# Kernel tuning notes

Measured on AMD Instinct MI355X. Metric: run time of the kernel, lower is better.

Reference implementation:

```python
import jax, jax.numpy as jnp
import numpy as np

K = 5  # Chebyshev order


def laplacian(w):
    # normalized Laplacian: I - D^{-1/2} W D^{-1/2}
    d = jnp.sum(w, axis=1)
    d_re = 1.0 / jnp.sqrt(d + 1e-5)
    return jnp.eye(w.shape[0], dtype=w.dtype) - d_re[:, None] * w * d_re[None, :]


def cheb_terms(x, lap, k):
    # x: [B,N,C], lap: [N,N] -> [B,k,N,C]
    # Faithful to torch code: T0 = ones, then (x, lap@x) recurrence for k>2.
    t0 = jnp.ones_like(x)
    if k == 1:
        return t0[:, None]
    t1 = jnp.matmul(lap, x)
    if k == 2:
        return jnp.stack([t0, t1], axis=1)
    terms = [t0, x, t1]
    tkm1, tk = x, t1
    for _ in range(3, k):
        tkm1, tk = tk, 2.0 * jnp.matmul(lap, tk) - tkm1
        terms.append(tk)
    return jnp.stack(terms, axis=1)


def graph_conv(x, lap, w, k):
    # torch: cp.permute(0,2,3,1).flatten(2) @ w, i.e. flat index = c*k + t
    t = cheb_terms(x, lap, k)                       # [B,k,N,C]
    C = x.shape[-1]
    O = w.shape[-1]
    return jnp.einsum('bknc,cko->bno', t, w.reshape(C, k, O))


def setup_inputs() -> dict:
    key = jax.random.key(0)
    ks = jax.random.split(key, 9)
    B, N, Cin, H = 8192, 32, 60, 128
    return {
        'x': jax.random.normal(ks[0], (B, N, Cin), dtype=jnp.float32),
        'adj': jax.random.normal(ks[1], (N, N), dtype=jnp.float32) * 0.1,
        'adj_bias': jax.random.normal(ks[2], (1,), dtype=jnp.float32) * 0.1 + 0.2,
        'w1': jax.random.normal(ks[3], (K * Cin, H), dtype=jnp.float32) * 0.05,
        'b1': jax.random.normal(ks[4], (1, 1, H), dtype=jnp.float32) * 0.05,
        'w2': jax.random.normal(ks[5], (K * H, H), dtype=jnp.float32) * 0.05,
        'b2': jax.random.normal(ks[6], (1, 1, H), dtype=jnp.float32) * 0.05,
        'fc_w': jax.random.normal(ks[7], (2, N * H), dtype=jnp.float32) * 0.02,
        'fc_b': jax.random.normal(ks[8], (2,), dtype=jnp.float32) * 0.02,
    }


def reference(x, adj, adj_bias, w1, b1, w2, b2, fc_w, fc_b):
    # DGCNN.forward (eval mode: dropout = identity)
    a = jax.nn.relu(adj + adj_bias)
    lap = laplacian(a)
    h = graph_conv(x, lap, w1, K)
    h = jax.nn.relu(h + b1)      # B1ReLU
    h = graph_conv(h, lap, w2, K)
    h = jax.nn.relu(h + b2)
    h = h.reshape(h.shape[0], -1)  # [B, N*H]
    return h @ fc_w.T + fc_b
```

## Files before the change

### kernel.cpp

```cpp
#include <hip/hip_runtime.h>

typedef unsigned short u16;
typedef unsigned int u32;
typedef short bf16x8 __attribute__((ext_vector_type(8)));
typedef float f32x4 __attribute__((ext_vector_type(4)));

#define MFMA16(a, b, c) __builtin_amdgcn_mfma_f32_16x16x32_bf16((a), (b), (c), 0, 0, 0)

__device__ __forceinline__ u16 f2bf(float f) {
  u32 u = __builtin_bit_cast(u32, f);
  u += 0x7FFFu + ((u >> 16) & 1u);
  return (u16)(u >> 16);
}
__device__ __forceinline__ u32 pk2bf(float a, float b) {
#if __has_builtin(__builtin_amdgcn_cvt_pk_bf16_f32)
  auto v = __builtin_amdgcn_cvt_pk_bf16_f32(a, b);
  return __builtin_bit_cast(u32, v);
#else
  return (u32)f2bf(a) | ((u32)f2bf(b) << 16);
#endif
}

#define WS_MGF   0
#define WS_WT1F  8192
#define WS_WT2F  73728
#define WS_B1    204800
#define WS_B2    205312

__global__ void prep_kernel(const float* __restrict__ adj,
                            const float* __restrict__ adj_bias,
                            const float* __restrict__ w1,
                            const float* __restrict__ b1,
                            const float* __restrict__ w2,
                            const float* __restrict__ b2,
                            char* __restrict__ ws) {
  const int tid = threadIdx.x;
  if (blockIdx.x == 0) {
    __shared__ float sa[1024], Ls[1024], L2s[1024], L3s[1024], sdre[32];
    float bias = adj_bias[0];
    for (int i = tid; i < 1024; i += 256) sa[i] = fmaxf(adj[i] + bias, 0.0f);
    __syncthreads();
    if (tid < 32) {
      float s = 0.0f;
      for (int c = 0; c < 32; ++c) s += sa[tid * 32 + c];
      sdre[tid] = 1.0f / sqrtf(s + 1e-5f);
    }
    __syncthreads();
    for (int i = tid; i < 1024; i += 256) {
      int n = i >> 5, c = i & 31;
      Ls[i] = (n == c ? 1.0f : 0.0f) - sdre[n] * sa[i] * sdre[c];
    }
    __syncthreads();
    for (int i = tid; i < 1024; i += 256) {
      int r = i >> 5, c = i & 31;
      float s = 0.0f;
      for (int m = 0; m < 32; ++m) s += Ls[r * 32 + m] * Ls[m * 32 + c];
      L2s[i] = s;
    }
    __syncthreads();
    for (int i = tid; i < 1024; i += 256) {
      int r = i >> 5, c = i & 31;
      float s = 0.0f;
      for (int m = 0; m < 32; ++m) s += L2s[r * 32 + m] * Ls[m * 32 + c];
      L3s[i] = s;
    }
    __syncthreads();
    u16* MGf = (u16*)(ws + WS_MGF);
    for (int i = tid; i < 4096; i += 256) {
      int jt = i >> 9, lane = (i >> 3) & 63, j = i & 7;
      int col = jt * 16 + (lane & 15);
      int k = ((lane >> 4) << 3) + j;
      int kk = col >> 5, np = col & 31;
      float v;
      if (kk == 0)      v = (np == k) ? 1.0f : 0.0f;
      else if (kk == 1) v = Ls[np * 32 + k];
      else if (kk == 2) v = 2.0f * L2s[np * 32 + k] - (np == k ? 1.0f : 0.0f);
      else              v = 4.0f * L3s[np * 32 + k] - 3.0f * Ls[np * 32 + k];
      MGf[i] = f2bf(v);
    }
    float* B1 = (float*)(ws + WS_B1);
    float* B2 = (float*)(ws + WS_B2);
    if (tid < 128) {
      float s = b1[tid];
      for (int c = 0; c < 60; ++c) s += w1[(c * 5) * 128 + tid];
      B1[tid] = s;
    } else {
      int o = tid - 128;
      float s = b2[o];
      for (int c = 0; c < 128; ++c) s += w2[(c * 5) * 128 + o];
      B2[o] = s;
    }
  } else {
    u16* WT1F = (u16*)(ws + WS_WT1F);
    u16* WT2F = (u16*)(ws + WS_WT2F);
    int g = (blockIdx.x - 1) * 256 + tid;
    for (int i = g; i < 32768; i += 16 * 256) {
      int ot = i >> 12, ks = (i >> 9) & 7, lane = (i >> 3) & 63, j = i & 7;
      int o = ot * 16 + (lane & 15);
      int kc = ks * 32 + ((lane >> 4) << 3) + j;
      int k = kc >> 6, c = kc & 63;
      WT1F[i] = (c < 60) ? f2bf(w1[(c * 5 + k + 1) * 128 + o]) : (u16)0;
    }
    for (int i = g; i < 65536; i += 16 * 256) {
      int mt = i >> 13, h = (i >> 12) & 1, ks = (i >> 9) & 7;
      int lane = (i >> 3) & 63, j = i & 7;
      int kc = ((ks >> 1) << 7) + ((ks & 1) << 5) + (h << 6) + (((lane >> 4)) << 3) + j;
      int k = kc >> 7, c = kc & 127;
      int o = (mt << 4) + (lane & 15);
      WT2F[i] = f2bf(w2[(c * 5 + k + 1) * 128 + o]);
    }
  }
}

__global__ __launch_bounds__(256, 5) void dgcnn_kernel(
    const float* __restrict__ x,
    const char* __restrict__ ws,
    const float* __restrict__ fc_w,
    const float* __restrict__ fc_b,
    float* __restrict__ out) {
  __shared__ __align__(16) char arena[27136];
  __shared__ float red[8];
  u16* Xt = (u16*)arena;
  u16* Ht = (u16*)arena;
  u16* Y  = (u16*)(arena + 10240);

  const u16* MGf  = (const u16*)(ws + WS_MGF);
  const u16* WT1F = (const u16*)(ws + WS_WT1F);
  const u16* WT2F = (const u16*)(ws + WS_WT2F);
  const float* bias1 = (const float*)(ws + WS_B1);
  const float* bias2 = (const float*)(ws + WS_B2);

  const int tid = threadIdx.x;
  const int w = tid >> 6, lane = tid & 63;
  const int l15 = lane & 15, q = lane >> 4;
  const int b = blockIdx.x;
  const f32x4 z4 = {0.0f, 0.0f, 0.0f, 0.0f};

  for (int i = tid; i < 160; i += 256) Xt[(60 + (i / 40)) * 40 + (i % 40)] = 0;
  bf16x8 mB0 = *(const bf16x8*)(MGf + ((2 * w + 0) * 64 + lane) * 8);
  bf16x8 mB1 = *(const bf16x8*)(MGf + ((2 * w + 1) * 64 + lane) * 8);
  const float* xb = x + (size_t)b * 1920;
  for (int i = tid; i < 1920; i += 256) {
    int n = i / 60, c = i - n * 60;
    Xt[c * 40 + n] = f2bf(xb[i]);
  }
  __syncthreads();

  {
    f32x4 acc[4][2];
#pragma unroll
    for (int mt = 0; mt < 4; ++mt) {
      bf16x8 aX = *(const bf16x8*)&Xt[(mt * 16 + l15) * 40 + q * 8];
      acc[mt][0] = MFMA16(aX, mB0, z4);
      acc[mt][1] = MFMA16(aX, mB1, z4);
    }
    __syncthreads();
#pragma unroll
    for (int mt = 0; mt < 4; ++mt)
#pragma unroll
      for (int jt = 0; jt < 2; ++jt) {
        int np = jt * 16 + l15;
        uint2 vv;
        vv.x = pk2bf(acc[mt][jt][0], acc[mt][jt][1]);
        vv.y = pk2bf(acc[mt][jt][2], acc[mt][jt][3]);
        *(uint2*)&Y[np * 264 + w * 64 + mt * 16 + q * 4] = vv;
      }
  }
  __syncthreads();

  {
    f32x4 acc[2][2] = {{z4, z4}, {z4, z4}};
#pragma unroll
    for (int ks = 0; ks < 8; ++ks) {
      bf16x8 a0 = *(const bf16x8*)&Y[(l15) * 264 + ks * 32 + q * 8];
      bf16x8 a1 = *(const bf16x8*)&Y[(16 + l15) * 264 + ks * 32 + q * 8];
      bf16x8 b0 = *(const bf16x8*)(WT1F + (((2 * w + 0) * 8 + ks) * 64 + lane) * 8);
      bf16x8 b1 = *(const bf16x8*)(WT1F + (((2 * w + 1) * 8 + ks) * 64 + lane) * 8);
      acc[0][0] = MFMA16(a0, b0, acc[0][0]);
      acc[0][1] = MFMA16(a0, b1, acc[0][1]);
      acc[1][0] = MFMA16(a1, b0, acc[1][0]);
      acc[1][1] = MFMA16(a1, b1, acc[1][1]);
    }
#pragma unroll
    for (int ot = 0; ot < 2; ++ot) {
      int o = (2 * w + ot) * 16 + l15;
      float bv = bias1[o];
#pragma unroll
      for (int mt = 0; mt < 2; ++mt) {
        uint2 vv;
        vv.x = pk2bf(fmaxf(acc[mt][ot][0] + bv, 0.0f), fmaxf(acc[mt][ot][1] + bv, 0.0f));
        vv.y = pk2bf(fmaxf(acc[mt][ot][2] + bv, 0.0f), fmaxf(acc[mt][ot][3] + bv, 0.0f));
        *(uint2*)&Ht[o * 40 + mt * 16 + q * 4] = vv;
      }
    }
  }
  __syncthreads();

  f32x4 acc2[2][2] = {{z4, z4}, {z4, z4}};
#pragma unroll
  for (int h = 0; h < 2; ++h) {
    {
      f32x4 acc[4][2];
#pragma unroll
      for (int mtl = 0; mtl < 4; ++mtl) {
        int mt = 4 * h + mtl;
        bf16x8 aH = *(const bf16x8*)&Ht[(mt * 16 + l15) * 40 + q * 8];
        acc[mtl][0] = MFMA16(aH, mB0, z4);
        acc[mtl][1] = MFMA16(aH, mB1, z4);
      }
#pragma unroll
      for (int mtl = 0; mtl < 4; ++mtl)
#pragma unroll
        for (int jt = 0; jt < 2; ++jt) {
          int np = jt * 16 + l15;
          uint2 vv;
          vv.x = pk2bf(acc[mtl][jt][0], acc[mtl][jt][1]);
          vv.y = pk2bf(acc[mtl][jt][2], acc[mtl][jt][3]);
          *(uint2*)&Y[np * 264 + w * 64 + mtl * 16 + q * 4] = vv;
        }
    }
    __syncthreads();
#pragma unroll
    for (int ks = 0; ks < 8; ++ks) {
      bf16x8 aw0 = *(const bf16x8*)(WT2F + ((((2 * w + 0) * 2 + h) * 8 + ks) * 64 + lane) * 8);
      bf16x8 aw1 = *(const bf16x8*)(WT2F + ((((2 * w + 1) * 2 + h) * 8 + ks) * 64 + lane) * 8);
      bf16x8 by0 = *(const bf16x8*)&Y[(l15) * 264 + ks * 32 + q * 8];
      bf16x8 by1 = *(const bf16x8*)&Y[(16 + l15) * 264 + ks * 32 + q * 8];
      acc2[0][0] = MFMA16(aw0, by0, acc2[0][0]);
      acc2[0][1] = MFMA16(aw0, by1, acc2[0][1]);
      acc2[1][0] = MFMA16(aw1, by0, acc2[1][0]);
      acc2[1][1] = MFMA16(aw1, by1, acc2[1][1]);
    }
    __syncthreads();
  }

  float p0 = 0.0f, p1 = 0.0f;
#pragma unroll
  for (int ot = 0; ot < 2; ++ot) {
    int ob = (2 * w + ot) * 16 + q * 4;
    float4 bv = *(const float4*)&bias2[ob];
#pragma unroll
    for (int nt = 0; nt < 2; ++nt) {
      int n = nt * 16 + l15;
      float h0 = fmaxf(acc2[ot][nt][0] + bv.x, 0.0f);
      float h1 = fmaxf(acc2[ot][nt][1] + bv.y, 0.0f);
      float h2 = fmaxf(acc2[ot][nt][2] + bv.z, 0.0f);
      float h3 = fmaxf(acc2[ot][nt][3] + bv.w, 0.0f);
      float4 w0 = *(const float4*)&fc_w[n * 128 + ob];
      float4 w1v = *(const float4*)&fc_w[4096 + n * 128 + ob];
      p0 = fmaf(h0, w0.x, fmaf(h1, w0.y, fmaf(h2, w0.z, fmaf(h3, w0.w, p0))));
      p1 = fmaf(h0, w1v.x, fmaf(h1, w1v.y, fmaf(h2, w1v.z, fmaf(h3, w1v.w, p1))));
    }
  }
#pragma unroll
  for (int off = 32; off >= 1; off >>= 1) {
    p0 += __shfl_xor(p0, off);
    p1 += __shfl_xor(p1, off);
  }
  if (lane == 0) {
    red[w * 2 + 0] = p0;
    red[w * 2 + 1] = p1;
  }
  __syncthreads();
  if (tid < 2) {
    out[b * 2 + tid] = red[tid] + red[2 + tid] + red[4 + tid] + red[6 + tid] + fc_b[tid];
  }
}

extern "C" void kernel_launch(void* const* d_in, const int* in_sizes, int n_in,
                              void* d_out, int out_size, void* d_ws, size_t ws_size,
                              hipStream_t stream) {
  const float* x        = (const float*)d_in[0];
  const float* adj      = (const float*)d_in[1];
  const float* adj_bias = (const float*)d_in[2];
  const float* w1       = (const float*)d_in[3];
  const float* b1       = (const float*)d_in[4];
  const float* w2       = (const float*)d_in[5];
  const float* b2       = (const float*)d_in[6];
  const float* fc_w     = (const float*)d_in[7];
  const float* fc_b     = (const float*)d_in[8];
  float* out = (float*)d_out;
  char* ws   = (char*)d_ws;

  prep_kernel<<<17, 256, 0, stream>>>(adj, adj_bias, w1, b1, w2, b2, ws);
  dgcnn_kernel<<<8192, 256, 0, stream>>>(x, ws, fc_w, fc_b, out);
}
```

Before: 206.4 us.

## Use two-wave blocks with wider per-wave output tiles and K-chunked Y staging

Shrinks each block from four waves to two, so each wave owns four output tiles and keeps four graph-operator fragments in registers. The Y staging buffer becomes a smaller K-chunk (32 nodes by 128 columns, split into halves or quarters) that is refilled and consumed in a loop, and the weight fragment layout in the prep kernel is re-swizzled to match. LDS use per block drops and row paddings change, aiming at more resident blocks per CU and fewer idle waves at barriers. In exchange there are more barrier rounds per block, higher register pressure from the larger accumulator arrays, and fewer threads to load x.

```diff
diff --git a/kernel.cpp b/kernel.cpp
--- a/kernel.cpp
+++ b/kernel.cpp
@@ -95,34 +95,35 @@
     u16* WT2F = (u16*)(ws + WS_WT2F);
     int g = (blockIdx.x - 1) * 256 + tid;
     for (int i = g; i < 32768; i += 16 * 256) {
-      int ot = i >> 12, ks = (i >> 9) & 7, lane = (i >> 3) & 63, j = i & 7;
+      int j = i & 7, lane = (i >> 3) & 63, ks = (i >> 9) & 3;
+      int h = (i >> 11) & 1, ot = i >> 12;
+      int q = lane >> 4;
+      int c = h * 32 + q * 8 + j;
       int o = ot * 16 + (lane & 15);
-      int kc = ks * 32 + ((lane >> 4) << 3) + j;
-      int k = kc >> 6, c = kc & 63;
-      WT1F[i] = (c < 60) ? f2bf(w1[(c * 5 + k + 1) * 128 + o]) : (u16)0;
+      WT1F[i] = (c < 60) ? f2bf(w1[(c * 5 + ks + 1) * 128 + o]) : (u16)0;
     }
     for (int i = g; i < 65536; i += 16 * 256) {
-      int mt = i >> 13, h = (i >> 12) & 1, ks = (i >> 9) & 7;
-      int lane = (i >> 3) & 63, j = i & 7;
-      int kc = ((ks >> 1) << 7) + ((ks & 1) << 5) + (h << 6) + (((lane >> 4)) << 3) + j;
-      int k = kc >> 7, c = kc & 127;
-      int o = (mt << 4) + (lane & 15);
-      WT2F[i] = f2bf(w2[(c * 5 + k + 1) * 128 + o]);
-    }
-  }
-}
-
-__global__ __launch_bounds__(256, 5) void dgcnn_kernel(
+      int j = i & 7, lane = (i >> 3) & 63, ks = (i >> 9) & 3;
+      int h = (i >> 11) & 3, mt = i >> 13;
+      int q = lane >> 4;
+      int c2 = h * 32 + q * 8 + j;
+      int o = mt * 16 + (lane & 15);
+      WT2F[i] = f2bf(w2[(c2 * 5 + ks + 1) * 128 + o]);
+    }
+  }
+}
+
+__global__ __launch_bounds__(128, 4) void dgcnn_kernel(
     const float* __restrict__ x,
     const char* __restrict__ ws,
     const float* __restrict__ fc_w,
     const float* __restrict__ fc_b,
     float* __restrict__ out) {
-  __shared__ __align__(16) char arena[27136];
-  __shared__ float red[8];
+  __shared__ __align__(16) char arena[18560];
+  __shared__ float red[4];
   u16* Xt = (u16*)arena;
   u16* Ht = (u16*)arena;
-  u16* Y  = (u16*)(arena + 10240);
+  u16* Y  = (u16*)(arena + 9728);
 
   const u16* MGf  = (const u16*)(ws + WS_MGF);
   const u16* WT1F = (const u16*)(ws + WS_WT1F);
@@ -136,118 +137,127 @@
   const int b = blockIdx.x;
   const f32x4 z4 = {0.0f, 0.0f, 0.0f, 0.0f};
 
-  for (int i = tid; i < 160; i += 256) Xt[(60 + (i / 40)) * 40 + (i % 40)] = 0;
-  bf16x8 mB0 = *(const bf16x8*)(MGf + ((2 * w + 0) * 64 + lane) * 8);
-  bf16x8 mB1 = *(const bf16x8*)(MGf + ((2 * w + 1) * 64 + lane) * 8);
+  bf16x8 mB[4];
+#pragma unroll
+  for (int t = 0; t < 4; ++t)
+    mB[t] = *(const bf16x8*)(MGf + ((4 * w + t) * 64 + lane) * 8);
+
+  {
+    int r = 60 + (tid >> 5), col = tid & 31;
+    Xt[r * 42 + col] = 0;
+  }
   const float* xb = x + (size_t)b * 1920;
-  for (int i = tid; i < 1920; i += 256) {
+  for (int i = tid; i < 1920; i += 128) {
     int n = i / 60, c = i - n * 60;
-    Xt[c * 40 + n] = f2bf(xb[i]);
+    Xt[c * 42 + n] = f2bf(xb[i]);
   }
   __syncthreads();
 
-  {
-    f32x4 acc[4][2];
-#pragma unroll
-    for (int mt = 0; mt < 4; ++mt) {
-      bf16x8 aX = *(const bf16x8*)&Xt[(mt * 16 + l15) * 40 + q * 8];
-      acc[mt][0] = MFMA16(aX, mB0, z4);
-      acc[mt][1] = MFMA16(aX, mB1, z4);
-    }
-    __syncthreads();
-#pragma unroll
-    for (int mt = 0; mt < 4; ++mt)
-#pragma unroll
-      for (int jt = 0; jt < 2; ++jt) {
-        int np = jt * 16 + l15;
-        uint2 vv;
-        vv.x = pk2bf(acc[mt][jt][0], acc[mt][jt][1]);
-        vv.y = pk2bf(acc[mt][jt][2], acc[mt][jt][3]);
-        *(uint2*)&Y[np * 264 + w * 64 + mt * 16 + q * 4] = vv;
-      }
-  }
-  __syncthreads();
-
-  {
-    f32x4 acc[2][2] = {{z4, z4}, {z4, z4}};
-#pragma unroll
-    for (int ks = 0; ks < 8; ++ks) {
-      bf16x8 a0 = *(const bf16x8*)&Y[(l15) * 264 + ks * 32 + q * 8];
-      bf16x8 a1 = *(const bf16x8*)&Y[(16 + l15) * 264 + ks * 32 + q * 8];
-      bf16x8 b0 = *(const bf16x8*)(WT1F + (((2 * w + 0) * 8 + ks) * 64 + lane) * 8);
-      bf16x8 b1 = *(const bf16x8*)(WT1F + (((2 * w + 1) * 8 + ks) * 64 + lane) * 8);
-      acc[0][0] = MFMA16(a0, b0, acc[0][0]);
-      acc[0][1] = MFMA16(a0, b1, acc[0][1]);
-      acc[1][0] = MFMA16(a1, b0, acc[1][0]);
-      acc[1][1] = MFMA16(a1, b1, acc[1][1]);
-    }
-#pragma unroll
-    for (int ot = 0; ot < 2; ++ot) {
-      int o = (2 * w + ot) * 16 + l15;
-      float bv = bias1[o];
-#pragma unroll
-      for (int mt = 0; mt < 2; ++mt) {
-        uint2 vv;
-        vv.x = pk2bf(fmaxf(acc[mt][ot][0] + bv, 0.0f), fmaxf(acc[mt][ot][1] + bv, 0.0f));
-        vv.y = pk2bf(fmaxf(acc[mt][ot][2] + bv, 0.0f), fmaxf(acc[mt][ot][3] + bv, 0.0f));
-        *(uint2*)&Ht[o * 40 + mt * 16 + q * 4] = vv;
-      }
-    }
-  }
-  __syncthreads();
-
-  f32x4 acc2[2][2] = {{z4, z4}, {z4, z4}};
+  f32x4 acc1[4][2] = {{z4, z4}, {z4, z4}, {z4, z4}, {z4, z4}};
 #pragma unroll
   for (int h = 0; h < 2; ++h) {
     {
-      f32x4 acc[4][2];
-#pragma unroll
-      for (int mtl = 0; mtl < 4; ++mtl) {
-        int mt = 4 * h + mtl;
-        bf16x8 aH = *(const bf16x8*)&Ht[(mt * 16 + l15) * 40 + q * 8];
-        acc[mtl][0] = MFMA16(aH, mB0, z4);
-        acc[mtl][1] = MFMA16(aH, mB1, z4);
-      }
-#pragma unroll
-      for (int mtl = 0; mtl < 4; ++mtl)
-#pragma unroll
-        for (int jt = 0; jt < 2; ++jt) {
-          int np = jt * 16 + l15;
-          uint2 vv;
-          vv.x = pk2bf(acc[mtl][jt][0], acc[mtl][jt][1]);
-          vv.y = pk2bf(acc[mtl][jt][2], acc[mtl][jt][3]);
-          *(uint2*)&Y[np * 264 + w * 64 + mtl * 16 + q * 4] = vv;
-        }
-    }
-    __syncthreads();
-#pragma unroll
-    for (int ks = 0; ks < 8; ++ks) {
-      bf16x8 aw0 = *(const bf16x8*)(WT2F + ((((2 * w + 0) * 2 + h) * 8 + ks) * 64 + lane) * 8);
-      bf16x8 aw1 = *(const bf16x8*)(WT2F + ((((2 * w + 1) * 2 + h) * 8 + ks) * 64 + lane) * 8);
-      bf16x8 by0 = *(const bf16x8*)&Y[(l15) * 264 + ks * 32 + q * 8];
-      bf16x8 by1 = *(const bf16x8*)&Y[(16 + l15) * 264 + ks * 32 + q * 8];
-      acc2[0][0] = MFMA16(aw0, by0, acc2[0][0]);
-      acc2[0][1] = MFMA16(aw0, by1, acc2[0][1]);
-      acc2[1][0] = MFMA16(aw1, by0, acc2[1][0]);
-      acc2[1][1] = MFMA16(aw1, by1, acc2[1][1]);
-    }
-    __syncthreads();
+      bf16x8 aX0 = *(const bf16x8*)&Xt[((2 * h + 0) * 16 + l15) * 42 + q * 8];
+      bf16x8 aX1 = *(const bf16x8*)&Xt[((2 * h + 1) * 16 + l15) * 42 + q * 8];
+#pragma unroll
+      for (int ktl = 0; ktl < 2; ++ktl) {
+        f32x4 g00 = MFMA16(aX0, mB[2 * ktl + 0], z4);
+        f32x4 g01 = MFMA16(aX0, mB[2 * ktl + 1], z4);
+        f32x4 g10 = MFMA16(aX1, mB[2 * ktl + 0], z4);
+        f32x4 g11 = MFMA16(aX1, mB[2 * ktl + 1], z4);
+        int cb = (2 * w + ktl) * 32 + q * 4;
+        uint2 v;
+        v.x = pk2bf(g00[0], g00[1]); v.y = pk2bf(g00[2], g00[3]);
+        *(uint2*)&Y[l15 * 138 + cb] = v;
+        v.x = pk2bf(g01[0], g01[1]); v.y = pk2bf(g01[2], g01[3]);
+        *(uint2*)&Y[(16 + l15) * 138 + cb] = v;
+        v.x = pk2bf(g10[0], g10[1]); v.y = pk2bf(g10[2], g10[3]);
+        *(uint2*)&Y[l15 * 138 + cb + 16] = v;
+        v.x = pk2bf(g11[0], g11[1]); v.y = pk2bf(g11[2], g11[3]);
+        *(uint2*)&Y[(16 + l15) * 138 + cb + 16] = v;
+      }
+    }
+    __syncthreads();
+#pragma unroll
+    for (int ks = 0; ks < 4; ++ks) {
+      bf16x8 a0 = *(const bf16x8*)&Y[l15 * 138 + ks * 32 + q * 8];
+      bf16x8 a1 = *(const bf16x8*)&Y[(16 + l15) * 138 + ks * 32 + q * 8];
+#pragma unroll
+      for (int ot = 0; ot < 4; ++ot) {
+        bf16x8 wf = *(const bf16x8*)(WT1F + ((((4 * w + ot) * 2 + h) * 4 + ks) * 64 + lane) * 8);
+        acc1[ot][0] = MFMA16(a0, wf, acc1[ot][0]);
+        acc1[ot][1] = MFMA16(a1, wf, acc1[ot][1]);
+      }
+    }
+    if (h == 0) __syncthreads();
+  }
+#pragma unroll
+  for (int ot = 0; ot < 4; ++ot) {
+    int o = (4 * w + ot) * 16 + l15;
+    float bv = bias1[o];
+#pragma unroll
+    for (int nt = 0; nt < 2; ++nt) {
+      uint2 v;
+      v.x = pk2bf(fmaxf(acc1[ot][nt][0] + bv, 0.0f), fmaxf(acc1[ot][nt][1] + bv, 0.0f));
+      v.y = pk2bf(fmaxf(acc1[ot][nt][2] + bv, 0.0f), fmaxf(acc1[ot][nt][3] + bv, 0.0f));
+      *(uint2*)&Ht[o * 38 + nt * 16 + q * 4] = v;
+    }
+  }
+  __syncthreads();
+
+  f32x4 acc2[4][2] = {{z4, z4}, {z4, z4}, {z4, z4}, {z4, z4}};
+#pragma unroll
+  for (int hh = 0; hh < 4; ++hh) {
+    {
+      bf16x8 aH0 = *(const bf16x8*)&Ht[((2 * hh + 0) * 16 + l15) * 38 + q * 8];
+      bf16x8 aH1 = *(const bf16x8*)&Ht[((2 * hh + 1) * 16 + l15) * 38 + q * 8];
+#pragma unroll
+      for (int ktl = 0; ktl < 2; ++ktl) {
+        f32x4 g00 = MFMA16(aH0, mB[2 * ktl + 0], z4);
+        f32x4 g01 = MFMA16(aH0, mB[2 * ktl + 1], z4);
+        f32x4 g10 = MFMA16(aH1, mB[2 * ktl + 0], z4);
+        f32x4 g11 = MFMA16(aH1, mB[2 * ktl + 1], z4);
+        int cb = (2 * w + ktl) * 32 + q * 4;
+        uint2 v;
+        v.x = pk2bf(g00[0], g00[1]); v.y = pk2bf(g00[2], g00[3]);
+        *(uint2*)&Y[l15 * 138 + cb] = v;
+        v.x = pk2bf(g01[0], g01[1]); v.y = pk2bf(g01[2], g01[3]);
+        *(uint2*)&Y[(16 + l15) * 138 + cb] = v;
+        v.x = pk2bf(g10[0], g10[1]); v.y = pk2bf(g10[2], g10[3]);
+        *(uint2*)&Y[l15 * 138 + cb + 16] = v;
+        v.x = pk2bf(g11[0], g11[1]); v.y = pk2bf(g11[2], g11[3]);
+        *(uint2*)&Y[(16 + l15) * 138 + cb + 16] = v;
+      }
+    }
+    __syncthreads();
+#pragma unroll
+    for (int ks = 0; ks < 4; ++ks) {
+      bf16x8 by0 = *(const bf16x8*)&Y[l15 * 138 + ks * 32 + q * 8];
+      bf16x8 by1 = *(const bf16x8*)&Y[(16 + l15) * 138 + ks * 32 + q * 8];
+#pragma unroll
+      for (int ot = 0; ot < 4; ++ot) {
+        bf16x8 aw = *(const bf16x8*)(WT2F + ((((4 * w + ot) * 4 + hh) * 4 + ks) * 64 + lane) * 8);
+        acc2[ot][0] = MFMA16(aw, by0, acc2[ot][0]);
+        acc2[ot][1] = MFMA16(aw, by1, acc2[ot][1]);
+      }
+    }
+    if (hh < 3) __syncthreads();
   }
 
   float p0 = 0.0f, p1 = 0.0f;
 #pragma unroll
-  for (int ot = 0; ot < 2; ++ot) {
-    int ob = (2 * w + ot) * 16 + q * 4;
+  for (int ot = 0; ot < 4; ++ot) {
+    int ob = (4 * w + ot) * 16 + q * 4;
     float4 bv = *(const float4*)&bias2[ob];
 #pragma unroll
     for (int nt = 0; nt < 2; ++nt) {
       int n = nt * 16 + l15;
+      float4 w0 = *(const float4*)&fc_w[n * 128 + ob];
+      float4 w1v = *(const float4*)&fc_w[4096 + n * 128 + ob];
       float h0 = fmaxf(acc2[ot][nt][0] + bv.x, 0.0f);
       float h1 = fmaxf(acc2[ot][nt][1] + bv.y, 0.0f);
       float h2 = fmaxf(acc2[ot][nt][2] + bv.z, 0.0f);
       float h3 = fmaxf(acc2[ot][nt][3] + bv.w, 0.0f);
-      float4 w0 = *(const float4*)&fc_w[n * 128 + ob];
-      float4 w1v = *(const float4*)&fc_w[4096 + n * 128 + ob];
       p0 = fmaf(h0, w0.x, fmaf(h1, w0.y, fmaf(h2, w0.z, fmaf(h3, w0.w, p0))));
       p1 = fmaf(h0, w1v.x, fmaf(h1, w1v.y, fmaf(h2, w1v.z, fmaf(h3, w1v.w, p1))));
     }
@@ -263,7 +273,7 @@
   }
   __syncthreads();
   if (tid < 2) {
-    out[b * 2 + tid] = red[tid] + red[2 + tid] + red[4 + tid] + red[6 + tid] + fc_b[tid];
+    out[b * 2 + tid] = red[tid] + red[2 + tid] + fc_b[tid];
   }
 }
 
@@ -283,5 +293,5 @@
   char* ws   = (char*)d_ws;
 
   prep_kernel<<<17, 256, 0, stream>>>(adj, adj_bias, w1, b1, w2, b2, ws);
-  dgcnn_kernel<<<8192, 256, 0, stream>>>(x, ws, fc_w, fc_b, out);
-}
+  dgcnn_kernel<<<8192, 128, 0, stream>>>(x, ws, fc_w, fc_b, out);
+}
```

Result: slower. 324.4 us (+57.2%).
